# Kernel tuning notes

Hardware: AMD Instinct MI355X
Metric: run time of the kernel (lower is better)

The kernel has to match this reference:

```python
import jax, jax.numpy as jnp
import numpy as np

WS = 512   # window_size
LB = 1     # look_backward
LF = 1     # look_forward
H = 16     # num_attention_heads
NC = LB + LF + 1  # concatenated windows per query window


def _collect(a, pad_value):
    # a: [B, nw, ws, ...]; gather windows [i-LB, i+LF] for each window i,
    # padding the window axis with pad_value (faithful to collect_windows).
    nw = a.shape[1]
    pads = [(0, 0), (LB, LF)] + [(0, 0)] * (a.ndim - 2)
    ap = jnp.pad(a, pads, constant_values=pad_value)
    idx = jnp.arange(nw)[:, None] + jnp.arange(NC)[None, :]  # [nw, NC]
    g = ap[:, idx]  # [B, nw, NC, ws, ...]
    return g.reshape(g.shape[0], nw, NC * a.shape[2], *a.shape[3:])


def setup_inputs() -> dict:
    key = jax.random.key(0)
    ks = jax.random.split(key, 9)
    B, S, E = 1, 4096, 1024
    x = jax.random.normal(ks[0], (B, S, E), dtype=jnp.float32)
    std = 0.02
    wq = std * jax.random.normal(ks[1], (E, E), dtype=jnp.float32)
    wk = std * jax.random.normal(ks[2], (E, E), dtype=jnp.float32)
    wv = std * jax.random.normal(ks[3], (E, E), dtype=jnp.float32)
    wo = std * jax.random.normal(ks[4], (E, E), dtype=jnp.float32)
    bq = std * jax.random.normal(ks[5], (E,), dtype=jnp.float32)
    bk = std * jax.random.normal(ks[6], (E,), dtype=jnp.float32)
    bv = std * jax.random.normal(ks[7], (E,), dtype=jnp.float32)
    bo = std * jax.random.normal(ks[8], (E,), dtype=jnp.float32)
    return {"x": x, "wq": wq, "bq": bq, "wk": wk, "bk": bk,
            "wv": wv, "bv": bv, "wo": wo, "bo": bo}


def reference(x, wq, bq, wk, bk, wv, bv, wo, bo):
    B, S, E = x.shape
    hd = E // H
    nw = S // WS  # seq_len chosen divisible by window_size

    def proj(w, b):
        y = x @ w.T + b
        return y.reshape(B, S, H, hd).transpose(0, 2, 1, 3).reshape(B * H, S, hd)

    q = proj(wq, bq)
    k = proj(wk, bk)
    v = proj(wv, bv)

    qb = q.reshape(B * H, nw, WS, hd)
    # NOTE: original pads K/V window buffers with value -1 (not zero); pad
    # positions are NOT masked (the `!= -1` clause excludes them) -- replicated.
    kb = _collect(k.reshape(B * H, nw, WS, hd), -1.0)  # [BH, nw, NC*WS, hd]
    vb = _collect(v.reshape(B * H, nw, WS, hd), -1.0)

    t = jnp.arange(S, dtype=jnp.int32).reshape(1, nw, WS)
    ct = _collect(t, -1)  # [1, nw, NC*WS] key positions (-1 for pads)

    # Unscaled QK^T (original applies no 1/sqrt(d)).
    scores = jnp.einsum('bwqd,bwkd->bwqk', qb, kb)  # [BH, nw, WS, NC*WS]

    qi = t.reshape(1, nw, WS, 1)          # query absolute positions
    ctb = ct[:, :, None, :]               # key absolute positions
    over = ((ctb > qi + WS * LF) | (ctb < qi - WS * LB)) & (ctb != -1)
    scores = jnp.where(over, -jnp.inf, scores)

    attn = jax.nn.softmax(scores, axis=-1)
    out = jnp.einsum('bwqk,bwkd->bwqd', attn, vb)  # [BH, nw, WS, hd]
    out = out.reshape(B, H, S, hd).transpose(0, 2, 1, 3).reshape(B, S, E)
    return out @ wo.T + bo
```

## Files before the change

### kernel.cpp

```cpp
#include <hip/hip_runtime.h>
#include <stdint.h>

#define S 4096
#define E 1024
#define NH 16
#define HD 64
#define WSZ 512

typedef _Float16 f16x8 __attribute__((ext_vector_type(8)));
typedef _Float16 f16x4 __attribute__((ext_vector_type(4)));
typedef float f32x4 __attribute__((ext_vector_type(4)));
typedef unsigned short u16;
typedef unsigned int u32;

__device__ __forceinline__ u16 f2h_bits(float f) {
    union { _Float16 h; u16 u; } cv; cv.h = (_Float16)f; return cv.u;
}

__device__ __forceinline__ void gld16(const u16* g, u16* l) {
    __builtin_amdgcn_global_load_lds((const __attribute__((address_space(1))) void*)g,
                                     (__attribute__((address_space(3))) void*)l, 16, 0, 0);
}

struct CvtArgs {
    const float* s[5];
    u16* d[5];
    int n[5];
};
__global__ void cvt5(CvtArgs a) {
    int seg = blockIdx.y;
    const float* __restrict__ s = a.s[seg];
    u16* __restrict__ d = a.d[seg];
    int n = a.n[seg];
    for (int i = (blockIdx.x * 256 + threadIdx.x) * 4; i < n; i += gridDim.x * 1024) {
        float4 f = *(const float4*)&s[i];
        uint2 o;
        o.x = (u32)f2h_bits(f.x) | ((u32)f2h_bits(f.y) << 16);
        o.y = (u32)f2h_bits(f.z) | ((u32)f2h_bits(f.w) << 16);
        *(uint2*)&d[i] = o;
    }
}

__global__ __launch_bounds__(256) void gemm_qkv(
    const u16* __restrict__ A, const u16* __restrict__ B,
    u16* __restrict__ OutQK, u16* __restrict__ OutVT,
    const float* __restrict__ b0, const float* __restrict__ b1, const float* __restrict__ b2,
    int K) {
    __shared__ __align__(16) u16 As[2 * 128 * 32];
    __shared__ __align__(16) u16 Bs[2 * 128 * 32];
    const int tid = threadIdx.x;
    const int wid = tid >> 6, lid = tid & 63, quad = lid >> 4, l16 = lid & 15;
    const int wm = wid >> 1, wn = wid & 1;
    const int bm0 = blockIdx.x * 128, bn0 = blockIdx.y * 128;

    f32x4 acc[4][4] = {};
    const int srow = tid >> 2, scol = (tid & 3) * 8;

    for (int k0 = 0; k0 < K; k0 += 64) {
        __syncthreads();
#pragma unroll
        for (int half = 0; half < 2; ++half)
#pragma unroll
            for (int rep = 0; rep < 2; ++rep) {
                gld16(&A[(size_t)(bm0 + rep * 64 + srow) * K + k0 + half * 32 + scol],
                      &As[half * 4096 + rep * 2048 + tid * 8]);
                gld16(&B[(size_t)(bn0 + rep * 64 + srow) * K + k0 + half * 32 + scol],
                      &Bs[half * 4096 + rep * 2048 + tid * 8]);
            }
        __syncthreads();
#pragma unroll
        for (int kk = 0; kk < 2; ++kk) {
            f16x8 af[4], bf[4];
#pragma unroll
            for (int i = 0; i < 4; ++i) af[i] = *(const f16x8*)&As[kk * 4096 + (wm * 64 + i * 16 + l16) * 32 + quad * 8];
#pragma unroll
            for (int j = 0; j < 4; ++j) bf[j] = *(const f16x8*)&Bs[kk * 4096 + (wn * 64 + j * 16 + l16) * 32 + quad * 8];
#pragma unroll
            for (int i = 0; i < 4; ++i)
#pragma unroll
                for (int j = 0; j < 4; ++j)
                    acc[i][j] = __builtin_amdgcn_mfma_f32_16x16x32_f16(af[i], bf[j], acc[i][j], 0, 0, 0);
        }
    }

    const bool isV = (bn0 >= 2048);
#pragma unroll
    for (int j = 0; j < 4; ++j) {
        int n = bn0 + wn * 64 + j * 16 + l16;
        float bias = (n < 1024) ? b0[n] : (n < 2048 ? b1[n - 1024] : b2[n - 2048]);
#pragma unroll
        for (int i = 0; i < 4; ++i) {
            int m0 = bm0 + wm * 64 + i * 16 + quad * 4;
            if (!isV) {
#pragma unroll
                for (int r = 0; r < 4; ++r)
                    OutQK[(size_t)(m0 + r) * 2048 + n] = f2h_bits(acc[i][j][r] + bias);
            } else {
                u16 h0 = f2h_bits(acc[i][j][0] + bias);
                u16 h1 = f2h_bits(acc[i][j][1] + bias);
                u16 h2 = f2h_bits(acc[i][j][2] + bias);
                u16 h3 = f2h_bits(acc[i][j][3] + bias);
                uint2 pk;
                pk.x = (u32)h0 | ((u32)h1 << 16);
                pk.y = (u32)h2 | ((u32)h3 << 16);
                *(uint2*)&OutVT[(size_t)(n - 2048) * 4096 + m0] = pk;
            }
        }
    }
}

__global__ __launch_bounds__(256) void gemm_n64(
    const u16* __restrict__ A, const u16* __restrict__ B, float* __restrict__ OutF,
    const float* __restrict__ bias, int N, int K) {
    __shared__ __align__(16) u16 As[2 * 128 * 32];
    __shared__ __align__(16) u16 Bs[2 * 64 * 32];
    const int tid = threadIdx.x;
    const int wid = tid >> 6, lid = tid & 63, quad = lid >> 4, l16 = lid & 15;
    const int bm0 = blockIdx.x * 128, bn0 = blockIdx.y * 64;

    f32x4 acc[2][4] = {};
    const int srow = tid >> 2, scol = (tid & 3) * 8;

    for (int k0 = 0; k0 < K; k0 += 64) {
        __syncthreads();
#pragma unroll
        for (int half = 0; half < 2; ++half) {
#pragma unroll
            for (int rep = 0; rep < 2; ++rep)
                gld16(&A[(size_t)(bm0 + rep * 64 + srow) * K + k0 + half * 32 + scol],
                      &As[half * 4096 + rep * 2048 + tid * 8]);
            gld16(&B[(size_t)(bn0 + srow) * K + k0 + half * 32 + scol],
                  &Bs[half * 2048 + tid * 8]);
        }
        __syncthreads();
#pragma unroll
        for (int kk = 0; kk < 2; ++kk) {
            f16x8 af[2], bf[4];
#pragma unroll
            for (int i = 0; i < 2; ++i) af[i] = *(const f16x8*)&As[kk * 4096 + (wid * 32 + i * 16 + l16) * 32 + quad * 8];
#pragma unroll
            for (int j = 0; j < 4; ++j) bf[j] = *(const f16x8*)&Bs[kk * 2048 + (j * 16 + l16) * 32 + quad * 8];
#pragma unroll
            for (int i = 0; i < 2; ++i)
#pragma unroll
                for (int j = 0; j < 4; ++j)
                    acc[i][j] = __builtin_amdgcn_mfma_f32_16x16x32_f16(af[i], bf[j], acc[i][j], 0, 0, 0);
        }
    }

#pragma unroll
    for (int j = 0; j < 4; ++j) {
        int n = bn0 + j * 16 + l16;
        float bv = bias[n];
#pragma unroll
        for (int i = 0; i < 2; ++i) {
            int m0 = bm0 + wid * 32 + i * 16 + quad * 4;
#pragma unroll
            for (int r = 0; r < 4; ++r)
                OutF[(size_t)(m0 + r) * N + n] = acc[i][j][r] + bv;
        }
    }
}

__global__ __launch_bounds__(512, 2) void attn_win(const u16* __restrict__ QK, const u16* __restrict__ VT,
                                                   u16* __restrict__ AO) {
    const int qt = blockIdx.x, w = blockIdx.y, h = blockIdx.z;
    const int tid = threadIdx.x, wid = tid >> 6, lid = tid & 63, quad = lid >> 4, l16 = lid & 15;

    __shared__ __align__(16) u16 Ks[2][2 * 128 * 32];
    __shared__ __align__(16) u16 Vt[2][4 * 64 * 36];

    const int qrow = w * WSZ + qt * 128 + wid * 16 + l16;
    const _Float16 L2E = (_Float16)1.44269504f;
    f16x8 qf[2];
#pragma unroll
    for (int ks = 0; ks < 2; ++ks) {
        qf[ks] = *(const f16x8*)&QK[(size_t)qrow * 2048 + h * 64 + ks * 32 + quad * 8];
#pragma unroll
        for (int j = 0; j < 8; ++j) qf[ks][j] *= L2E;
    }

    const int npad = (w == 0 || w == 7) ? 512 : 0;
    float s_p = 0.f;
    if (npad) {
        float sq = 0.f;
#pragma unroll
        for (int j = 0; j < 8; ++j) sq += (float)qf[0][j] + (float)qf[1][j];
        sq += __shfl_xor(sq, 16, 64);
        sq += __shfl_xor(sq, 32, 64);
        s_p = -sq;
    }

    f32x4 oacc[4] = {};
    float mrun = -30000.f;
    float lsum = 0.f;

    const int g0base = (w - 1) * WSZ;
    const int rqloc = qt * 128 + wid * 16 + l16;
    const int rqw0 = qt * 128 + wid * 16;

    int cfirst = 2 * qt; if ((1 - w) * 8 > cfirst) cfirst = (1 - w) * 8;
    int clast = 2 * qt + 17; if (71 - 8 * w < clast) clast = 71 - 8 * w; if (clast > 23) clast = 23;

    const int krow = tid >> 2;
    const size_t kg = 1024 + h * 64 + (tid & 3) * 8;
    const int kl = tid * 8;
    const int vd = tid >> 3, vk0 = (tid & 7) * 16;
    const u16* vgrow = VT + (size_t)(h * 64 + vd) * 4096;
    const int vloff = (vk0 >> 5) * 2304 + vd * 36 + (vk0 & 31);

    {
        const int g0 = g0base + cfirst * 64;
        uint4 va = *(const uint4*)(vgrow + g0 + vk0);
        uint4 vb = *(const uint4*)(vgrow + g0 + vk0 + 8);
        gld16(QK + (size_t)(g0 + krow) * 2048 + kg,      &Ks[0][kl]);
        gld16(QK + (size_t)(g0 + krow) * 2048 + kg + 32, &Ks[0][4096 + kl]);
        u16* vp = &Vt[0][vloff];
        *(uint2*)(vp)      = make_uint2(va.x, va.y);
        *(uint2*)(vp + 4)  = make_uint2(va.z, va.w);
        *(uint2*)(vp + 8)  = make_uint2(vb.x, vb.y);
        *(uint2*)(vp + 12) = make_uint2(vb.z, vb.w);
    }

    int ib = 0;
    for (int c0 = cfirst; c0 <= clast; c0 += 2, ib ^= 1) {
        __syncthreads();

        const bool has_next = (c0 + 2 <= clast);
        uint4 vna, vnb;
        if (has_next) {
            const int gn = g0base + (c0 + 2) * 64;
            vna = *(const uint4*)(vgrow + gn + vk0);
            vnb = *(const uint4*)(vgrow + gn + vk0 + 8);
            gld16(QK + (size_t)(gn + krow) * 2048 + kg,      &Ks[ib ^ 1][kl]);
            gld16(QK + (size_t)(gn + krow) * 2048 + kg + 32, &Ks[ib ^ 1][4096 + kl]);
        }

        const u16* KsB = &Ks[ib][0];
        const u16* VtB = &Vt[ib][0];
        const int ncs = (c0 + 1 <= clast) ? 2 : 1;

#pragma unroll
        for (int cs = 0; cs < 2; ++cs) {
            if (cs >= ncs) break;
            const int c = c0 + cs;

            f32x4 sc[4];
#pragma unroll
            for (int nt = 0; nt < 4; ++nt) {
                f16x8 kf0 = *(const f16x8*)&KsB[(cs * 64 + nt * 16 + l16) * 32 + quad * 8];
                f16x8 kf1 = *(const f16x8*)&KsB[4096 + (cs * 64 + nt * 16 + l16) * 32 + quad * 8];
                f32x4 t = {};
                t = __builtin_amdgcn_mfma_f32_16x16x32_f16(kf0, qf[0], t, 0, 0, 0);
                t = __builtin_amdgcn_mfma_f32_16x16x32_f16(kf1, qf[1], t, 0, 0, 0);
                sc[nt] = t;
            }

            const bool needs_mask = (c * 64 < rqw0 + 16) || (c * 64 + 63 > rqw0 + 1024);
            if (needs_mask) {
#pragma unroll
                for (int nt = 0; nt < 4; ++nt)
#pragma unroll
                    for (int r = 0; r < 4; ++r) {
                        int n = c * 64 + nt * 16 + quad * 4 + r;
                        if (n < rqloc || n > rqloc + 1024) sc[nt][r] = -30000.f;
                    }
            }

            float mloc = mrun;
#pragma unroll
            for (int nt = 0; nt < 4; ++nt)
                mloc = fmaxf(mloc, fmaxf(fmaxf(sc[nt][0], sc[nt][1]), fmaxf(sc[nt][2], sc[nt][3])));
            mloc = fmaxf(mloc, __shfl_xor(mloc, 16, 64));
            mloc = fmaxf(mloc, __shfl_xor(mloc, 32, 64));

            const bool up = __any(mloc > mrun);
            float ls = 0.f;
            f16x4 pf[4];
#pragma unroll
            for (int nt = 0; nt < 4; ++nt)
#pragma unroll
                for (int r = 0; r < 4; ++r) {
                    float p = exp2f(sc[nt][r] - mloc);
                    ls += p;
                    pf[nt][r] = (_Float16)p;
                }
            if (up) {
                float alpha = exp2f(mrun - mloc);
                mrun = mloc;
                lsum = lsum * alpha + ls;
                float ao[4];
#pragma unroll
                for (int r = 0; r < 4; ++r) ao[r] = __shfl(alpha, quad * 4 + r, 64);
#pragma unroll
                for (int dt = 0; dt < 4; ++dt)
#pragma unroll
                    for (int r = 0; r < 4; ++r) oacc[dt][r] *= ao[r];
            } else {
                lsum += ls;
            }

#pragma unroll
            for (int nt = 0; nt < 4; ++nt)
#pragma unroll
                for (int dt = 0; dt < 4; ++dt) {
                    f16x4 vf = *(const f16x4*)&VtB[(cs * 2 + (nt >> 1)) * 2304 + (dt * 16 + l16) * 36 + (nt & 1) * 16 + quad * 4];
                    oacc[dt] = __builtin_amdgcn_mfma_f32_16x16x16f16(pf[nt], vf, oacc[dt], 0, 0, 0);
                }
        }

        if (has_next) {
            u16* vp = &Vt[ib ^ 1][vloff];
            *(uint2*)(vp)      = make_uint2(vna.x, vna.y);
            *(uint2*)(vp + 4)  = make_uint2(vna.z, vna.w);
            *(uint2*)(vp + 8)  = make_uint2(vnb.x, vnb.y);
            *(uint2*)(vp + 12) = make_uint2(vnb.z, vnb.w);
        }
    }

    float lt = lsum;
    lt += __shfl_xor(lt, 16, 64);
    lt += __shfl_xor(lt, 32, 64);
    float aW = 1.f, pw = 0.f;
    if (npad) {
        float mnew = fmaxf(mrun, s_p);
        aW = exp2f(mrun - mnew);
        pw = 512.f * exp2f(s_p - mnew);
        lt = lt * aW + pw;
    }
    float linv = 1.f / lt;
    float lrec[4], arow[4], pwrow[4];
#pragma unroll
    for (int r = 0; r < 4; ++r) {
        lrec[r]  = __shfl(linv, quad * 4 + r, 64);
        arow[r]  = __shfl(aW,   quad * 4 + r, 64);
        pwrow[r] = __shfl(pw,   quad * 4 + r, 64);
    }
#pragma unroll
    for (int dt = 0; dt < 4; ++dt)
#pragma unroll
        for (int r = 0; r < 4; ++r) {
            int srow = w * WSZ + qt * 128 + wid * 16 + quad * 4 + r;
            int col = h * 64 + dt * 16 + l16;
            float o = (oacc[dt][r] * arow[r] - pwrow[r]) * lrec[r];
            AO[(size_t)srow * E + col] = f2h_bits(o);
        }
}

extern "C" void kernel_launch(void* const* d_in, const int* in_sizes, int n_in,
                              void* d_out, int out_size, void* d_ws, size_t ws_size,
                              hipStream_t stream) {
    const float* x  = (const float*)d_in[0];
    const float* wq = (const float*)d_in[1];
    const float* bq = (const float*)d_in[2];
    const float* wk = (const float*)d_in[3];
    const float* bk = (const float*)d_in[4];
    const float* wv = (const float*)d_in[5];
    const float* bv = (const float*)d_in[6];
    const float* wo = (const float*)d_in[7];
    const float* bo = (const float*)d_in[8];
    float* out = (float*)d_out;

    char* ws = (char*)d_ws;
    u16* XH  = (u16*)(ws);
    u16* WC  = (u16*)(ws + 8388608);
    u16* WOh = (u16*)(ws + 14680064);
    u16* QK  = (u16*)(ws + 16777216);
    u16* VTg = (u16*)(ws + 33554432);
    u16* AOh = (u16*)(ws + 41943040);

    CvtArgs ca;
    ca.s[0] = x;  ca.d[0] = XH;            ca.n[0] = 4194304;
    ca.s[1] = wq; ca.d[1] = WC;            ca.n[1] = 1048576;
    ca.s[2] = wk; ca.d[2] = WC + 1048576;  ca.n[2] = 1048576;
    ca.s[3] = wv; ca.d[3] = WC + 2097152;  ca.n[3] = 1048576;
    ca.s[4] = wo; ca.d[4] = WOh;           ca.n[4] = 1048576;
    cvt5<<<dim3(1024, 5), 256, 0, stream>>>(ca);

    gemm_qkv<<<dim3(32, 24), 256, 0, stream>>>(XH, WC, QK, VTg, bq, bk, bv, 1024);
    attn_win<<<dim3(4, 8, 16), 512, 0, stream>>>(QK, VTg, AOh);
    gemm_n64<<<dim3(32, 16), 256, 0, stream>>>(AOh, WOh, out, bo, 1024, 1024);
}
```

Before: 188.9 us.

## Remap GEMM block indices for XCD locality and stage V-transpose stores through LDS

The QKV and output-projection GEMMs now remap the flat block index so that blocks sharing the same A row tile and nearby B column tiles land together, which is intended to improve L2 reuse across the MI355X's chiplets. The V-transposed epilogue in the QKV GEMM now writes the tile into padded shared memory and then emits coalesced 16-byte row stores, replacing scattered 8-byte stores. Shared memory grows to hold the padded transpose buffer, and the remap hardcodes the grid shape (32 by 24 and 32 by 16).

```diff
diff --git a/kernel.cpp b/kernel.cpp
--- a/kernel.cpp
+++ b/kernel.cpp
@@ -46,12 +46,15 @@
     u16* __restrict__ OutQK, u16* __restrict__ OutVT,
     const float* __restrict__ b0, const float* __restrict__ b1, const float* __restrict__ b2,
     int K) {
-    __shared__ __align__(16) u16 As[2 * 128 * 32];
-    __shared__ __align__(16) u16 Bs[2 * 128 * 32];
+    __shared__ __align__(16) u16 SMEM[17408];
+    u16* As = SMEM;
+    u16* Bs = SMEM + 8192;
     const int tid = threadIdx.x;
     const int wid = tid >> 6, lid = tid & 63, quad = lid >> 4, l16 = lid & 15;
     const int wm = wid >> 1, wn = wid & 1;
-    const int bm0 = blockIdx.x * 128, bn0 = blockIdx.y * 128;
+    const int flat = blockIdx.x + 32 * blockIdx.y;
+    const int bm0 = ((flat >> 3) & 31) * 128;
+    const int bn0 = ((flat & 7) * 3 + (flat >> 8)) * 128;
 
     f32x4 acc[4][4] = {};
     const int srow = tid >> 2, scol = (tid & 3) * 8;
@@ -84,28 +87,40 @@
     }
 
     const bool isV = (bn0 >= 2048);
-#pragma unroll
-    for (int j = 0; j < 4; ++j) {
-        int n = bn0 + wn * 64 + j * 16 + l16;
-        float bias = (n < 1024) ? b0[n] : (n < 2048 ? b1[n - 1024] : b2[n - 2048]);
-#pragma unroll
-        for (int i = 0; i < 4; ++i) {
-            int m0 = bm0 + wm * 64 + i * 16 + quad * 4;
-            if (!isV) {
+    if (!isV) {
+#pragma unroll
+        for (int j = 0; j < 4; ++j) {
+            int n = bn0 + wn * 64 + j * 16 + l16;
+            float bias = (n < 1024) ? b0[n] : b1[n - 1024];
+#pragma unroll
+            for (int i = 0; i < 4; ++i) {
+                int m0 = bm0 + wm * 64 + i * 16 + quad * 4;
 #pragma unroll
                 for (int r = 0; r < 4; ++r)
                     OutQK[(size_t)(m0 + r) * 2048 + n] = f2h_bits(acc[i][j][r] + bias);
-            } else {
-                u16 h0 = f2h_bits(acc[i][j][0] + bias);
-                u16 h1 = f2h_bits(acc[i][j][1] + bias);
-                u16 h2 = f2h_bits(acc[i][j][2] + bias);
-                u16 h3 = f2h_bits(acc[i][j][3] + bias);
-                uint2 pk;
-                pk.x = (u32)h0 | ((u32)h1 << 16);
-                pk.y = (u32)h2 | ((u32)h3 << 16);
-                *(uint2*)&OutVT[(size_t)(n - 2048) * 4096 + m0] = pk;
-            }
-        }
+            }
+        }
+    } else {
+        __syncthreads();
+#pragma unroll
+        for (int j = 0; j < 4; ++j) {
+            const int n_l = wn * 64 + j * 16 + l16;
+            float bias = b2[bn0 - 2048 + n_l];
+#pragma unroll
+            for (int i = 0; i < 4; ++i) {
+                const int mbase = wm * 64 + i * 16 + quad * 4;
+#pragma unroll
+                for (int r = 0; r < 4; ++r)
+                    SMEM[n_l * 136 + mbase + r] = f2h_bits(acc[i][j][r] + bias);
+            }
+        }
+        __syncthreads();
+        const int n_l = tid >> 1, mh = (tid & 1) * 64;
+        u16* dst = OutVT + (size_t)(bn0 - 2048 + n_l) * 4096 + bm0 + mh;
+        const u16* src = &SMEM[n_l * 136 + mh];
+#pragma unroll
+        for (int t = 0; t < 8; ++t)
+            *(uint4*)(dst + t * 8) = *(const uint4*)(src + t * 8);
     }
 }
 
@@ -116,7 +131,9 @@
     __shared__ __align__(16) u16 Bs[2 * 64 * 32];
     const int tid = threadIdx.x;
     const int wid = tid >> 6, lid = tid & 63, quad = lid >> 4, l16 = lid & 15;
-    const int bm0 = blockIdx.x * 128, bn0 = blockIdx.y * 64;
+    const int flat = blockIdx.x + 32 * blockIdx.y;
+    const int bm0 = ((flat >> 3) & 31) * 128;
+    const int bn0 = ((flat & 7) * 2 + (flat >> 8)) * 64;
 
     f32x4 acc[2][4] = {};
     const int srow = tid >> 2, scol = (tid & 3) * 8;
```

Measured after the change: 208.1 us. 1.1x slower.
